# Kernel tuning notes

Measured on AMD Instinct MI355X. Metric: run time of the kernel, lower is better.

Reference implementation:

```python
import jax, jax.numpy as jnp
import numpy as np

N = 128 * 128          # hardcoded in the original forward: x.view(1, 1, 128*128)
SCORE_LIMIT = int(0.5 * N)   # int(score_limit * num_inputs) = 8192
K = 7                  # odd kernel_size, padding = K // 2 = 3


def setup_inputs() -> dict:
    key = jax.random.key(0)
    k1, k2 = jax.random.split(key)
    x = jax.random.normal(k1, (N,), dtype=jnp.float32)
    # Conv1d(1, 1, K, bias=False) weight, flattened to a length-K taps vector
    conv_w = jax.random.normal(k2, (K,), dtype=jnp.float32) * 0.1
    return {"x": x, "conv_w": conv_w}


def reference(x, conv_w):
    # torch Conv1d is cross-correlation with 'same' padding (K odd):
    # y[i] = sum_j w[j] * x[i + j - K//2]. jnp.convolve flips the kernel,
    # so pass conv_w reversed to get cross-correlation.
    y = jnp.convolve(x, conv_w[::-1], mode="same")
    attention_score = jax.nn.sigmoid(y)                     # [N]
    attention_index = jnp.argsort(attention_score)          # ascending, [N]
    keep = attention_index[:SCORE_LIMIT]                    # lowest-score indices kept (as in source)
    simple_score = attention_score[keep] + 1.0              # [SCORE_LIMIT]
    # zeros everywhere, scatter rescaled values at kept indices
    new_x = jnp.zeros_like(x).at[keep].set(x[keep] * simple_score)
    return new_x, attention_score
```

## Files before the change

kernel.cpp:

```cpp
#include <hip/hip_runtime.h>
#include <math.h>

#define N 16384
#define LIMIT 8192


__device__ __forceinline__ unsigned int score_bin(float s) {
    int d = (int)__float_as_uint(s) - 0x3E800000;
    int b = d >> 14;
    b = b < 0 ? 0 : (b > 1023 ? 1023 : b);
    return (unsigned int)b;
}

template <int W, int WIDTH>
__device__ __forceinline__ void scan_select(unsigned int* tot,
                                            unsigned int* partial,
                                            unsigned long long* prefix_sh,
                                            unsigned int* r_sh) {
    const int tid = threadIdx.x;
    const unsigned int r = *r_sh;
    if (tid < 256) {
        unsigned int p = 0;
#pragma unroll
        for (int q = 0; q < W / 4; ++q) {
            uint4 v = ((const uint4*)tot)[tid * (W / 4) + q];
            p += v.x + v.y + v.z + v.w;
        }
        partial[tid] = p;
    }
    __syncthreads();
    if (tid < 64) {
        unsigned int p0 = partial[4*tid+0], p1 = partial[4*tid+1],
                     p2 = partial[4*tid+2], p3 = partial[4*tid+3];
        const unsigned int g4 = p0 + p1 + p2 + p3;
        unsigned int incl = g4;
#pragma unroll
        for (int d = 1; d < 64; d <<= 1) {
            unsigned int up = __shfl_up(incl, d, 64);
            if (tid >= d) incl += up;
        }
        unsigned long long ball = __ballot(incl > r);
        int L = __ffsll((long long)ball) - 1;
        if (tid == L) {
            unsigned int cum = incl - g4;
            unsigned int pp[4] = {p0, p1, p2, p3};
            int grp = -1;
#pragma unroll
            for (int k = 0; k < 4; ++k)
                if (grp < 0) { if (cum + pp[k] > r) grp = 4*L + k; else cum += pp[k]; }
            unsigned int c[W];
#pragma unroll
            for (int q = 0; q < W / 4; ++q) {
                uint4 v = ((const uint4*)tot)[grp * (W / 4) + q];
                c[4*q+0] = v.x; c[4*q+1] = v.y; c[4*q+2] = v.z; c[4*q+3] = v.w;
            }
            int b = -1;
#pragma unroll
            for (int k = 0; k < W; ++k)
                if (b < 0) { if (cum + c[k] > r) b = grp * W + k; else cum += c[k]; }
            *r_sh = r - cum;
            *prefix_sh = (*prefix_sh << WIDTH) | (unsigned long long)b;
        }
    }
    __syncthreads();
}

__global__ __launch_bounds__(1024)
void fused16(const float* __restrict__ x, const float* __restrict__ w,
             float* __restrict__ out) {
    __shared__ __attribute__((aligned(16))) unsigned int h4[4096];
    __shared__ __attribute__((aligned(16))) unsigned int hist[1024];
    __shared__ __attribute__((aligned(16))) unsigned int partial[256];
    __shared__ __attribute__((aligned(16))) unsigned long long cand[2048];
    __shared__ __attribute__((aligned(16))) float haloR[16][4];
    __shared__ __attribute__((aligned(16))) float haloL[16][4];
    __shared__ unsigned long long prefix_sh, klT_sh;
    __shared__ unsigned int r_sh, cnt_sh;

    const int tid  = threadIdx.x;
    const int base = tid * 16;
    const int lane = tid & 63;
    const int wvi  = tid >> 6;

    float wv[7];
#pragma unroll
    for (int t = 0; t < 7; ++t) wv[t] = w[t];

    float xr[16];
    const float4* xv4 = (const float4*)x + tid * 4;
#pragma unroll
    for (int q = 0; q < 4; ++q) {
        float4 v = xv4[q];
        xr[4*q+0] = v.x; xr[4*q+1] = v.y; xr[4*q+2] = v.z; xr[4*q+3] = v.w;
    }

    float xm3 = __shfl_up(xr[13], 1, 64);
    float xm2 = __shfl_up(xr[14], 1, 64);
    float xm1 = __shfl_up(xr[15], 1, 64);
    float xp0 = __shfl_down(xr[0], 1, 64);
    float xp1 = __shfl_down(xr[1], 1, 64);
    float xp2 = __shfl_down(xr[2], 1, 64);

    if (lane == 63) { haloR[wvi][0] = xr[13]; haloR[wvi][1] = xr[14]; haloR[wvi][2] = xr[15]; }
    if (lane == 0)  { haloL[wvi][0] = xr[0];  haloL[wvi][1] = xr[1];  haloL[wvi][2] = xr[2];  }
    h4[tid] = 0; h4[tid+1024] = 0; h4[tid+2048] = 0; h4[tid+3072] = 0;
    if (tid == 0) { prefix_sh = 0ULL; r_sh = LIMIT - 1; cnt_sh = 0u; }
    __syncthreads();

    if (lane == 0) {
        if (wvi > 0) { xm3 = haloR[wvi-1][0]; xm2 = haloR[wvi-1][1]; xm1 = haloR[wvi-1][2]; }
        else         { xm3 = 0.f; xm2 = 0.f; xm1 = 0.f; }
    }
    if (lane == 63) {
        if (wvi < 15) { xp0 = haloL[wvi+1][0]; xp1 = haloL[wvi+1][1]; xp2 = haloL[wvi+1][2]; }
        else          { xp0 = 0.f; xp1 = 0.f; xp2 = 0.f; }
    }

    float win[22];
    win[0] = xm3; win[1] = xm2; win[2] = xm1;
#pragma unroll
    for (int k = 0; k < 16; ++k) win[3 + k] = xr[k];
    win[19] = xp0; win[20] = xp1; win[21] = xp2;

    float s[16];
#pragma unroll
    for (int k = 0; k < 16; ++k) {
        float acc = 0.f;
#pragma unroll
        for (int t = 0; t < 7; ++t)
            acc = __fadd_rn(acc, __fmul_rn(win[k + t], wv[t]));
        s[k] = 1.f / (1.f + expf(-acc));
    }

#pragma unroll
    for (int k = 0; k < 16; ++k) {
        const unsigned int b = score_bin(s[k]);
        atomicAdd(&h4[(b << 2) | (tid & 3)], 1u);
    }
    __syncthreads();

    hist[tid] = h4[4*tid] + h4[4*tid+1] + h4[4*tid+2] + h4[4*tid+3];
    __syncthreads();

    scan_select<4, 10>(hist, partial, &prefix_sh, &r_sh);
    const unsigned int b0 = (unsigned int)prefix_sh;
    const unsigned int r0 = r_sh;

#pragma unroll
    for (int k = 0; k < 16; ++k) {
        if (score_bin(s[k]) == b0) {
            unsigned int pos = atomicAdd(&cnt_sh, 1u);
            if (pos < 2048u)
                cand[pos] = ((unsigned long long)__float_as_uint(s[k]) << 14)
                            | (unsigned int)(base + k);
        }
    }
    __syncthreads();

    const unsigned int c = cnt_sh < 2048u ? cnt_sh : 2048u;
    for (unsigned int idx = tid; idx < c; idx += 1024) {
        unsigned long long v = cand[idx];
        unsigned int rk = 0;
        for (unsigned int j = 0; j < c; ++j) rk += (cand[j] < v) ? 1u : 0u;
        if (rk == r0) klT_sh = v;
    }
    __syncthreads();

    if (wvi == (int)blockIdx.x) {
        const unsigned long long T = klT_sh;
        float4* ov = (float4*)out + tid * 4;
        float4* so = (float4*)(out + N) + tid * 4;
#pragma unroll
        for (int q = 0; q < 4; ++q) {
            float4 o;
            float* op = &o.x;
#pragma unroll
            for (int e = 0; e < 4; ++e) {
                const float sk = s[4*q+e];
                const unsigned int bb = score_bin(sk);
                const unsigned long long key =
                    ((unsigned long long)__float_as_uint(sk) << 14)
                    | (unsigned int)(base + 4*q + e);
                const bool keep = (bb < b0) || ((bb == b0) && (key <= T));
                op[e] = keep ? __fmul_rn(win[3 + 4*q+e], __fadd_rn(sk, 1.0f)) : 0.f;
            }
            ov[q] = o;
            so[q] = make_float4(s[4*q+0], s[4*q+1], s[4*q+2], s[4*q+3]);
        }
    }
}

extern "C" void kernel_launch(void* const* d_in, const int* in_sizes, int n_in,
                              void* d_out, int out_size, void* d_ws, size_t ws_size,
                              hipStream_t stream) {
    (void)in_sizes; (void)n_in; (void)out_size; (void)d_ws; (void)ws_size;
    const float* x = (const float*)d_in[0];
    const float* w = (const float*)d_in[1];
    float* out = (float*)d_out;
    fused16<<<16, 1024, 0, stream>>>(x, w, out);
}
```

Before: 64.40 us.

## Stage scores in LDS so every block thread writes one output element

Each thread now writes its sigmoid scores to a padded LDS array instead of keeping 16 scores in registers. After the threshold is selected, all 1024 threads of every block write one element each, covering that block's 1024-element slice. Before, only one wave per block wrote 16 elements per thread. This spreads the final writes across the whole block and may lower register pressure, at the cost of about 65 KB more LDS, extra LDS traffic, and a global reload of x.

```diff
diff --git a/kernel.cpp b/kernel.cpp
--- a/kernel.cpp
+++ b/kernel.cpp
@@ -10,6 +10,10 @@
     int b = d >> 14;
     b = b < 0 ? 0 : (b > 1023 ? 1023 : b);
     return (unsigned int)b;
+}
+
+__device__ __forceinline__ int s_loc(int i) {
+    return (i & 15) * 1025 + (i >> 4);
 }
 
 template <int W, int WIDTH>
@@ -68,6 +72,7 @@
 __global__ __launch_bounds__(1024)
 void fused16(const float* __restrict__ x, const float* __restrict__ w,
              float* __restrict__ out) {
+    __shared__ __attribute__((aligned(16))) float s_lds[16 * 1025 + 64];
     __shared__ __attribute__((aligned(16))) unsigned int h4[4096];
     __shared__ __attribute__((aligned(16))) unsigned int hist[1024];
     __shared__ __attribute__((aligned(16))) unsigned int partial[256];
@@ -116,26 +121,24 @@
         else          { xp0 = 0.f; xp1 = 0.f; xp2 = 0.f; }
     }
 
-    float win[22];
-    win[0] = xm3; win[1] = xm2; win[2] = xm1;
+    {
+        float win[22];
+        win[0] = xm3; win[1] = xm2; win[2] = xm1;
 #pragma unroll
-    for (int k = 0; k < 16; ++k) win[3 + k] = xr[k];
-    win[19] = xp0; win[20] = xp1; win[21] = xp2;
-
-    float s[16];
-#pragma unroll
-    for (int k = 0; k < 16; ++k) {
-        float acc = 0.f;
-#pragma unroll
-        for (int t = 0; t < 7; ++t)
-            acc = __fadd_rn(acc, __fmul_rn(win[k + t], wv[t]));
-        s[k] = 1.f / (1.f + expf(-acc));
-    }
+        for (int k = 0; k < 16; ++k) win[3 + k] = xr[k];
+        win[19] = xp0; win[20] = xp1; win[21] = xp2;
 
 #pragma unroll
-    for (int k = 0; k < 16; ++k) {
-        const unsigned int b = score_bin(s[k]);
-        atomicAdd(&h4[(b << 2) | (tid & 3)], 1u);
+        for (int k = 0; k < 16; ++k) {
+            float acc = 0.f;
+#pragma unroll
+            for (int t = 0; t < 7; ++t)
+                acc = __fadd_rn(acc, __fmul_rn(win[k + t], wv[t]));
+            const float sk = 1.f / (1.f + expf(-acc));
+            s_lds[k * 1025 + tid] = sk;
+            const unsigned int b = score_bin(sk);
+            atomicAdd(&h4[(b << 2) | (tid & 3)], 1u);
+        }
     }
     __syncthreads();
 
@@ -148,10 +151,11 @@
 
 #pragma unroll
     for (int k = 0; k < 16; ++k) {
-        if (score_bin(s[k]) == b0) {
+        const float sk = s_lds[k * 1025 + tid];
+        if (score_bin(sk) == b0) {
             unsigned int pos = atomicAdd(&cnt_sh, 1u);
             if (pos < 2048u)
-                cand[pos] = ((unsigned long long)__float_as_uint(s[k]) << 14)
+                cand[pos] = ((unsigned long long)__float_as_uint(sk) << 14)
                             | (unsigned int)(base + k);
         }
     }
@@ -166,28 +170,15 @@
     }
     __syncthreads();
 
-    if (wvi == (int)blockIdx.x) {
-        const unsigned long long T = klT_sh;
-        float4* ov = (float4*)out + tid * 4;
-        float4* so = (float4*)(out + N) + tid * 4;
-#pragma unroll
-        for (int q = 0; q < 4; ++q) {
-            float4 o;
-            float* op = &o.x;
-#pragma unroll
-            for (int e = 0; e < 4; ++e) {
-                const float sk = s[4*q+e];
-                const unsigned int bb = score_bin(sk);
-                const unsigned long long key =
-                    ((unsigned long long)__float_as_uint(sk) << 14)
-                    | (unsigned int)(base + 4*q + e);
-                const bool keep = (bb < b0) || ((bb == b0) && (key <= T));
-                op[e] = keep ? __fmul_rn(win[3 + 4*q+e], __fadd_rn(sk, 1.0f)) : 0.f;
-            }
-            ov[q] = o;
-            so[q] = make_float4(s[4*q+0], s[4*q+1], s[4*q+2], s[4*q+3]);
-        }
-    }
+    const unsigned long long T = klT_sh;
+    const int g = blockIdx.x * 1024 + tid;
+    const float sk = s_lds[s_loc(g)];
+    const unsigned int bb = score_bin(sk);
+    const unsigned long long key = ((unsigned long long)__float_as_uint(sk) << 14)
+                                   | (unsigned int)g;
+    const bool keep = (bb < b0) || ((bb == b0) && (key <= T));
+    out[g]     = keep ? __fmul_rn(x[g], __fadd_rn(sk, 1.0f)) : 0.f;
+    out[N + g] = sk;
 }
 
 extern "C" void kernel_launch(void* const* d_in, const int* in_sizes, int n_in,
```

After: 63.06 us. 2.1% less time.
